# Kernel tuning notes

Measured on AMD Instinct MI355X. Metric: run time of the kernel, lower is better.

Reference implementation:

```python
import jax, jax.numpy as jnp
import numpy as np


def reference(x, edge_index, edge_attr, W, b):
    """PyG GCNConv: out = D^{-1/2} (A + I) D^{-1/2} X W + b.

    x: [N, Din] node features
    edge_index: [2, E] int (row=source, col=target)
    edge_attr: [E] edge weights
    W: [Din, Dout], b: [Dout]
    """
    N = x.shape[0]
    # add self-loops with weight 1 (PyG fill_value=1.0)
    loop = jnp.arange(N, dtype=edge_index.dtype)
    row = jnp.concatenate([edge_index[0], loop])
    col = jnp.concatenate([edge_index[1], loop])
    w = jnp.concatenate([edge_attr, jnp.ones((N,), dtype=edge_attr.dtype)])

    # symmetric normalization: norm_e = d[row]^-1/2 * w_e * d[col]^-1/2
    deg = jax.ops.segment_sum(w, col, num_segments=N)
    dis = jnp.where(deg > 0, jax.lax.rsqrt(jnp.where(deg > 0, deg, 1.0)), 0.0)
    norm = dis[row] * w * dis[col]

    # linear projection first (Din == Dout, cheaper either way), then
    # gather-scale-scatter aggregation at targets
    h = x @ W                                   # [N, Dout]
    msg = h[row] * norm[:, None]                # [E+N, Dout]
    out = jax.ops.segment_sum(msg, col, num_segments=N)  # [N, Dout]
    return out + b


def setup_inputs() -> dict:
    key = jax.random.key(0)
    k1, k2, k3, k4 = jax.random.split(key, 4)
    N, E, Din, Dout = 100000, 1600000, 128, 128
    x = jax.random.normal(k1, (N, Din), dtype=jnp.float32)
    edge_index = jax.random.randint(k2, (2, E), 0, N, dtype=jnp.int64)
    edge_attr = jax.random.uniform(k3, (E,), dtype=jnp.float32)
    # Glorot init like PyG Linear default
    W = jax.random.normal(k4, (Din, Dout), dtype=jnp.float32) * (1.0 / np.sqrt(Din))
    b = jnp.zeros((Dout,), dtype=jnp.float32)
    return {"x": x, "edge_index": edge_index, "edge_attr": edge_attr, "W": W, "b": b}
```

## Files before the change

kernel.cpp:

```cpp
#include <hip/hip_runtime.h>


#define ELEMS_PER_SCAN_BLOCK 4096
#define CHUNK 2048

typedef __attribute__((ext_vector_type(8))) short short8;
typedef __attribute__((ext_vector_type(4))) float f32x4;

__device__ inline unsigned short f2bf(float f) {
    unsigned u = __float_as_uint(f);
    u += 0x7fffu + ((u >> 16) & 1u);
    return (unsigned short)(u >> 16);
}
__device__ inline float bf_lo(unsigned u) { return __uint_as_float(u << 16); }
__device__ inline float bf_hi(unsigned u) { return __uint_as_float(u & 0xffff0000u); }

__global__ __launch_bounds__(256) void k_hist(const int* __restrict__ col,
                                              int* __restrict__ histg,
                                              int E, int NC, int NBLK) {
    __shared__ int lh[1024];
    int t = threadIdx.x, blk = blockIdx.x;
    for (int i = t; i < 1024; i += 256) lh[i] = 0;
    __syncthreads();
    int base = blk * CHUNK;
    #pragma unroll
    for (int i = 0; i < CHUNK / 256; ++i) {
        int e = base + i * 256 + t;
        if (e < E) atomicAdd(&lh[col[e] >> 7], 1);
    }
    __syncthreads();
    for (int b = t; b < NC; b += 256) histg[b * NBLK + blk] = lh[b];
}

__device__ inline int wave_incl_scan(int x, int lane) {
    #pragma unroll
    for (int d = 1; d < 64; d <<= 1) {
        int y = __shfl_up(x, d, 64);
        if (lane >= d) x += y;
    }
    return x;
}

__global__ void k_scan1(const int* __restrict__ in, int* __restrict__ out,
                        int* __restrict__ bsum, int M) {
    __shared__ int wsum[4];
    __shared__ int woff[4];
    int t = threadIdx.x, lane = t & 63, wid = t >> 6;
    int base = blockIdx.x * ELEMS_PER_SCAN_BLOCK + t * 16;
    int v[16];
    #pragma unroll
    for (int i = 0; i < 16; ++i) v[i] = (base + i < M) ? in[base + i] : 0;
    int run = 0;
    #pragma unroll
    for (int i = 0; i < 16; ++i) { int x = v[i]; v[i] = run; run += x; }
    int incl = wave_incl_scan(run, lane);
    int excl = incl - run;
    if (lane == 63) wsum[wid] = incl;
    __syncthreads();
    if (t == 0) {
        int r = 0;
        #pragma unroll
        for (int w = 0; w < 4; ++w) { int s = wsum[w]; woff[w] = r; r += s; }
        bsum[blockIdx.x] = r;
    }
    __syncthreads();
    int off = woff[wid] + excl;
    #pragma unroll
    for (int i = 0; i < 16; ++i)
        if (base + i < M) out[base + i] = v[i] + off;
}

__global__ void k_scan2(const int* __restrict__ bsum, int* __restrict__ boff, int NB) {
    __shared__ int wsum[4];
    __shared__ int woff[4];
    int t = threadIdx.x, lane = t & 63, wid = t >> 6;
    int x = (t < NB) ? bsum[t] : 0;
    int incl = wave_incl_scan(x, lane);
    int excl = incl - x;
    if (lane == 63) wsum[wid] = incl;
    __syncthreads();
    if (t == 0) {
        int r = 0;
        #pragma unroll
        for (int w = 0; w < 4; ++w) { int s = wsum[w]; woff[w] = r; r += s; }
    }
    __syncthreads();
    if (t < NB) boff[t] = woff[wid] + excl;
}

__global__ void k_scan3(int* __restrict__ arr, const int* __restrict__ boff, int M) {
    int t = threadIdx.x;
    int base = blockIdx.x * ELEMS_PER_SCAN_BLOCK + t * 16;
    int off = boff[blockIdx.x];
    #pragma unroll
    for (int i = 0; i < 16; ++i) {
        int idx = base + i;
        if (idx < M) arr[idx] += off;
    }
}

__global__ __launch_bounds__(256) void k_place(const int* __restrict__ row,
                                               const int* __restrict__ col,
                                               const float* __restrict__ wgt,
                                               const int* __restrict__ histg,
                                               int2* __restrict__ srw,
                                               int E, int NC, int NBLK) {
    __shared__ int lcnt[1024];
    __shared__ int gadj[1024];
    __shared__ int2 stage[CHUNK];
    __shared__ int sdst[CHUNK];
    __shared__ int wsum[4];
    __shared__ int woff[4];
    int t = threadIdx.x, blk = blockIdx.x;
    int lane = t & 63, wid = t >> 6;
    int base = blk * CHUNK;
    int nE = min(CHUNK, E - base);
    for (int b = t; b < 1024; b += 256) lcnt[b] = 0;
    __syncthreads();
    #pragma unroll
    for (int i = 0; i < CHUNK / 256; ++i) {
        int e = base + i * 256 + t;
        if (e < E) atomicAdd(&lcnt[col[e] >> 7], 1);
    }
    __syncthreads();
    int c4[4];
    int sum = 0;
    #pragma unroll
    for (int i = 0; i < 4; ++i) { int v = lcnt[t * 4 + i]; c4[i] = sum; sum += v; }
    int incl = wave_incl_scan(sum, lane);
    int excl = incl - sum;
    if (lane == 63) wsum[wid] = incl;
    __syncthreads();
    if (t == 0) {
        int r = 0;
        #pragma unroll
        for (int w = 0; w < 4; ++w) { int s = wsum[w]; woff[w] = r; r += s; }
    }
    __syncthreads();
    int tb = woff[wid] + excl;
    #pragma unroll
    for (int i = 0; i < 4; ++i) {
        int idx = t * 4 + i;
        int b0 = tb + c4[i];
        int gb = (idx < NC) ? histg[idx * NBLK + blk] : 0;
        gadj[idx] = gb - b0;
        lcnt[idx] = b0;
    }
    __syncthreads();
    #pragma unroll
    for (int i = 0; i < CHUNK / 256; ++i) {
        int e = base + i * 256 + t;
        if (e < E) {
            int c = col[e];
            int slot = atomicAdd(&lcnt[c >> 7], 1);
            stage[slot] = make_int2(((c & 127) << 17) | row[e], __float_as_int(wgt[e]));
            sdst[slot] = gadj[c >> 7] + slot;
        }
    }
    __syncthreads();
    for (int s_ = t; s_ < nE; s_ += 256) {
        srw[sdst[s_]] = stage[s_];
    }
}

__global__ __launch_bounds__(256) void k_fine(const int* __restrict__ histg,
                                              const int2* __restrict__ srw,
                                              int* __restrict__ rowptr,
                                              float* __restrict__ dis,
                                              int2* __restrict__ spack,
                                              int E, int N, int NC, int NBLK) {
    __shared__ int cnt128[128];
    __shared__ float degf[128];
    __shared__ int cur128[128];
    __shared__ int wtot[2];
    int t = threadIdx.x, b = blockIdx.x;
    int nb = b << 7;
    int start = histg[b * NBLK];
    int end = (b == NC - 1) ? E : histg[(b + 1) * NBLK];
    if (t < 128) { cnt128[t] = 0; degf[t] = 1.0f; }
    __syncthreads();
    for (int j = start + t; j < end; j += 256) {
        int2 s = srw[j];
        int c = s.x >> 17;
        atomicAdd(&cnt128[c], 1);
        atomicAdd(&degf[c], __int_as_float(s.y));
    }
    __syncthreads();
    int v = 0, incl = 0;
    if (t < 128) {
        v = cnt128[t];
        incl = wave_incl_scan(v, t & 63);
        if ((t & 63) == 63) wtot[t >> 6] = incl;
    }
    __syncthreads();
    if (t < 128) {
        int excl = incl - v + ((t >= 64) ? wtot[0] : 0);
        int p = start + excl;
        cur128[t] = p;
        int n = nb + t;
        if (n < N) {
            rowptr[n] = p;
            dis[n] = rsqrtf(degf[t]);
        }
    }
    if (t == 0 && b == NC - 1) rowptr[N] = E;
    __syncthreads();
    for (int j = start + t; j < end; j += 256) {
        int2 s = srw[j];
        int c = s.x >> 17;
        int pos = atomicAdd(&cur128[c], 1);
        spack[pos] = make_int2(s.x & 0x1FFFF, s.y);
    }
}

__global__ void k_wprep(const float* __restrict__ W, unsigned short* __restrict__ Wtg) {
    int n = blockIdx.x;
    int k = threadIdx.x;
    Wtg[n * 128 + k] = f2bf(W[k * 128 + n]);
}

__global__ __launch_bounds__(256) void k_gemm(const float* __restrict__ x,
                                              const unsigned short* __restrict__ Wtg,
                                              unsigned short* __restrict__ h, int N) {
    __shared__ short Xs[64][136];
    __shared__ short Ws[128][136];
    int t = threadIdx.x;
    int lane = t & 63, wid = t >> 6;
    int row0 = blockIdx.x * 64;
    {
        int r = t >> 2;
        int kseg = (t & 3) * 32;
        int gr = row0 + r;
        const float4* src = (const float4*)(x + (size_t)gr * 128 + kseg);
        #pragma unroll
        for (int i = 0; i < 4; ++i) {
            float4 v0 = make_float4(0.f, 0.f, 0.f, 0.f), v1 = v0;
            if (gr < N) { v0 = src[2 * i]; v1 = src[2 * i + 1]; }
            short8 p;
            p[0] = (short)f2bf(v0.x); p[1] = (short)f2bf(v0.y);
            p[2] = (short)f2bf(v0.z); p[3] = (short)f2bf(v0.w);
            p[4] = (short)f2bf(v1.x); p[5] = (short)f2bf(v1.y);
            p[6] = (short)f2bf(v1.z); p[7] = (short)f2bf(v1.w);
            *(short8*)&Xs[r][kseg + 8 * i] = p;
        }
    }
    {
        int n = t >> 1;
        int seg = (t & 1) * 64;
        const short* wsrc = (const short*)Wtg + n * 128 + seg;
        #pragma unroll
        for (int i = 0; i < 8; ++i)
            *(short8*)&Ws[n][seg + 8 * i] = *(const short8*)(wsrc + 8 * i);
    }
    __syncthreads();

    int q = lane >> 4;
    int m = lane & 15;
    f32x4 acc[8];
    #pragma unroll
    for (int tde = 0; tde < 8; ++tde) acc[tde] = (f32x4){0.f, 0.f, 0.f, 0.f};
    #pragma unroll
    for (int kc = 0; kc < 128; kc += 32) {
        short8 af = *(const short8*)&Xs[wid * 16 + m][kc + q * 8];
        #pragma unroll
        for (int tde = 0; tde < 8; ++tde) {
            short8 bf = *(const short8*)&Ws[tde * 16 + m][kc + q * 8];
            acc[tde] = __builtin_amdgcn_mfma_f32_16x16x32_bf16(af, bf, acc[tde], 0, 0, 0);
        }
    }
    #pragma unroll
    for (int r = 0; r < 4; ++r) {
        int grow = row0 + wid * 16 + q * 4 + r;
        if (grow < N) {
            #pragma unroll
            for (int tde = 0; tde < 8; ++tde)
                h[(size_t)grow * 128 + tde * 16 + m] = f2bf(acc[tde][r]);
        }
    }
}

__global__ __launch_bounds__(256) void k_gather(const unsigned int* __restrict__ hb,
                                                const float* __restrict__ dis,
                                                const int* __restrict__ rowptr,
                                                const long* __restrict__ spackl,
                                                const float* __restrict__ bias,
                                                float* __restrict__ out, int N) {
    int gid = blockIdx.x * blockDim.x + threadIdx.x;
    int node = gid >> 6;
    int lane = gid & 63;
    if (node >= N) return;
    node = __builtin_amdgcn_readfirstlane(node);

    float dn = dis[node];
    unsigned u = hb[(size_t)node * 64 + lane];
    float2 acc;
    acc.x = dn * bf_lo(u);
    acc.y = dn * bf_hi(u);

    int jb = rowptr[node], je = rowptr[node + 1];
    int j = jb;
    long q0, q1, q2, q3, q4, q5, q6, q7;
    if (j + 8 <= je) {
        q0 = __builtin_nontemporal_load(spackl + j);
        q1 = __builtin_nontemporal_load(spackl + j + 1);
        q2 = __builtin_nontemporal_load(spackl + j + 2);
        q3 = __builtin_nontemporal_load(spackl + j + 3);
        q4 = __builtin_nontemporal_load(spackl + j + 4);
        q5 = __builtin_nontemporal_load(spackl + j + 5);
        q6 = __builtin_nontemporal_load(spackl + j + 6);
        q7 = __builtin_nontemporal_load(spackl + j + 7);
    }
    for (; j + 8 <= je; j += 8) {
        int r0 = __builtin_amdgcn_readfirstlane((int)q0);
        int r1 = __builtin_amdgcn_readfirstlane((int)q1);
        int r2 = __builtin_amdgcn_readfirstlane((int)q2);
        int r3 = __builtin_amdgcn_readfirstlane((int)q3);
        int r4 = __builtin_amdgcn_readfirstlane((int)q4);
        int r5 = __builtin_amdgcn_readfirstlane((int)q5);
        int r6 = __builtin_amdgcn_readfirstlane((int)q6);
        int r7 = __builtin_amdgcn_readfirstlane((int)q7);
        unsigned u0 = hb[(size_t)r0 * 64 + lane];
        unsigned u1 = hb[(size_t)r1 * 64 + lane];
        unsigned u2 = hb[(size_t)r2 * 64 + lane];
        unsigned u3 = hb[(size_t)r3 * 64 + lane];
        unsigned u4 = hb[(size_t)r4 * 64 + lane];
        unsigned u5 = hb[(size_t)r5 * 64 + lane];
        unsigned u6 = hb[(size_t)r6 * 64 + lane];
        unsigned u7 = hb[(size_t)r7 * 64 + lane];
        int jn = (j + 16 <= je) ? j + 8 : j;
        long n0 = __builtin_nontemporal_load(spackl + jn);
        long n1 = __builtin_nontemporal_load(spackl + jn + 1);
        long n2 = __builtin_nontemporal_load(spackl + jn + 2);
        long n3 = __builtin_nontemporal_load(spackl + jn + 3);
        long n4 = __builtin_nontemporal_load(spackl + jn + 4);
        long n5 = __builtin_nontemporal_load(spackl + jn + 5);
        long n6 = __builtin_nontemporal_load(spackl + jn + 6);
        long n7 = __builtin_nontemporal_load(spackl + jn + 7);
        float a0 = dis[r0] * __uint_as_float((unsigned)((unsigned long)q0 >> 32));
        float a1 = dis[r1] * __uint_as_float((unsigned)((unsigned long)q1 >> 32));
        float a2 = dis[r2] * __uint_as_float((unsigned)((unsigned long)q2 >> 32));
        float a3 = dis[r3] * __uint_as_float((unsigned)((unsigned long)q3 >> 32));
        float a4 = dis[r4] * __uint_as_float((unsigned)((unsigned long)q4 >> 32));
        float a5 = dis[r5] * __uint_as_float((unsigned)((unsigned long)q5 >> 32));
        float a6 = dis[r6] * __uint_as_float((unsigned)((unsigned long)q6 >> 32));
        float a7 = dis[r7] * __uint_as_float((unsigned)((unsigned long)q7 >> 32));
        acc.x = fmaf(a0, bf_lo(u0), acc.x); acc.y = fmaf(a0, bf_hi(u0), acc.y);
        acc.x = fmaf(a1, bf_lo(u1), acc.x); acc.y = fmaf(a1, bf_hi(u1), acc.y);
        acc.x = fmaf(a2, bf_lo(u2), acc.x); acc.y = fmaf(a2, bf_hi(u2), acc.y);
        acc.x = fmaf(a3, bf_lo(u3), acc.x); acc.y = fmaf(a3, bf_hi(u3), acc.y);
        acc.x = fmaf(a4, bf_lo(u4), acc.x); acc.y = fmaf(a4, bf_hi(u4), acc.y);
        acc.x = fmaf(a5, bf_lo(u5), acc.x); acc.y = fmaf(a5, bf_hi(u5), acc.y);
        acc.x = fmaf(a6, bf_lo(u6), acc.x); acc.y = fmaf(a6, bf_hi(u6), acc.y);
        acc.x = fmaf(a7, bf_lo(u7), acc.x); acc.y = fmaf(a7, bf_hi(u7), acc.y);
        q0 = n0; q1 = n1; q2 = n2; q3 = n3; q4 = n4; q5 = n5; q6 = n6; q7 = n7;
    }
    for (; j < je; ++j) {
        long q = __builtin_nontemporal_load(spackl + j);
        int r = __builtin_amdgcn_readfirstlane((int)q);
        unsigned uu = hb[(size_t)r * 64 + lane];
        float a = dis[r] * __uint_as_float((unsigned)((unsigned long)q >> 32));
        acc.x = fmaf(a, bf_lo(uu), acc.x);
        acc.y = fmaf(a, bf_hi(uu), acc.y);
    }

    int c0 = lane * 2;
    float2 bv = *(const float2*)(bias + c0);
    float2 o;
    o.x = bv.x + dn * acc.x;
    o.y = bv.y + dn * acc.y;
    union { float2 f; double d; } cvt;
    cvt.f = o;
    __builtin_nontemporal_store(cvt.d, (double*)(out + (size_t)node * 128 + c0));
}

extern "C" void kernel_launch(void* const* d_in, const int* in_sizes, int n_in,
                              void* d_out, int out_size, void* d_ws, size_t ws_size,
                              hipStream_t stream) {
    const float* x     = (const float*)d_in[0];
    const int*   eidx  = (const int*)d_in[1];
    const float* eattr = (const float*)d_in[2];
    const float* W     = (const float*)d_in[3];
    const float* bias  = (const float*)d_in[4];
    int N = in_sizes[0] / 128;
    int E = in_sizes[2];
    const int* row = eidx;
    const int* col = eidx + E;

    int NC = (N + 127) >> 7;
    int NBLK = (E + CHUNK - 1) / CHUNK;

    char* p = (char*)d_ws;
    auto carve = [&](size_t bytes) {
        char* q = p;
        p += (bytes + 255) & ~(size_t)255;
        return q;
    };
    unsigned short* h   = (unsigned short*)carve((size_t)N * 128 * sizeof(unsigned short));
    unsigned short* Wtg = (unsigned short*)carve(128 * 128 * sizeof(unsigned short));
    float* dis    = (float*)carve((size_t)N * sizeof(float));
    int*   rowptr = (int*)carve((size_t)(N + 1) * sizeof(int));
    int*   histg  = (int*)carve((size_t)NC * NBLK * sizeof(int));
    int2*  srw    = (int2*)carve((size_t)E * sizeof(int2));
    int2*  spack  = (int2*)carve((size_t)E * sizeof(int2));
    int*   bsum   = (int*)carve(256 * sizeof(int));
    int*   boff   = (int*)carve(256 * sizeof(int));

    int M = NC * NBLK;
    int NBs = (M + ELEMS_PER_SCAN_BLOCK - 1) / ELEMS_PER_SCAN_BLOCK;

    k_hist<<<NBLK, 256, 0, stream>>>(col, histg, E, NC, NBLK);
    k_scan1<<<NBs, 256, 0, stream>>>(histg, histg, bsum, M);
    k_scan2<<<1, 256, 0, stream>>>(bsum, boff, NBs);
    k_scan3<<<NBs, 256, 0, stream>>>(histg, boff, M);
    k_place<<<NBLK, 256, 0, stream>>>(row, col, eattr, histg, srw, E, NC, NBLK);
    k_fine<<<NC, 256, 0, stream>>>(histg, srw, rowptr, dis, spack, E, N, NC, NBLK);
    k_wprep<<<128, 128, 0, stream>>>(W, Wtg);
    k_gemm<<<(N + 63) / 64, 256, 0, stream>>>(x, Wtg, h, N);
    {
        size_t threads = (size_t)N * 64;
        int blocks = (int)((threads + 255) / 256);
        k_gather<<<blocks, 256, 0, stream>>>((const unsigned int*)h, dis, rowptr,
                                             (const long*)spack, bias, (float*)d_out, N);
    }
}
```

Measured before the change: 270.2 us.

## Co-schedule GEMM blocks with CSR build kernels and fold scan and weight prep

The weight transpose and bf16 conversion move into the histogram kernel. The scan-offset add kernel is removed, and its block offsets are applied on the fly when the scanned histogram is read. Half of the GEMM tiles now run as extra blocks in the placement kernel and the other half in the fine-bucketing kernel, so the compute-bound projection overlaps with the memory- and atomic-bound CSR construction and the launch count drops. The fine kernel caches up to 3072 bucket entries in shared memory to avoid re-reading them from global memory. The union shared-memory layout raises per-block LDS, which may lower occupancy for the scatter phases.

```diff
diff --git a/kernel.cpp b/kernel.cpp
--- a/kernel.cpp
+++ b/kernel.cpp
@@ -2,6 +2,7 @@
 
 
 #define ELEMS_PER_SCAN_BLOCK 4096
+#define SCAN_SHIFT 12
 #define CHUNK 2048
 
 typedef __attribute__((ext_vector_type(8))) short short8;
@@ -15,11 +16,26 @@
 __device__ inline float bf_lo(unsigned u) { return __uint_as_float(u << 16); }
 __device__ inline float bf_hi(unsigned u) { return __uint_as_float(u & 0xffff0000u); }
 
+union SmemU {
+    struct { short Xs[64][136]; short Ws[128][136]; } g;
+    struct { int lcnt[1024]; int gadj[1024]; int2 stage[CHUNK]; int sdst[CHUNK];
+             int wsum[4]; int woff[4]; } p;
+    struct { int2 sbuf[3072]; int cnt128[128]; float degf[128]; int cur128[128];
+             int wtot[2]; } f;
+};
+
 __global__ __launch_bounds__(256) void k_hist(const int* __restrict__ col,
+                                              const float* __restrict__ W,
                                               int* __restrict__ histg,
+                                              unsigned short* __restrict__ Wtg,
                                               int E, int NC, int NBLK) {
     __shared__ int lh[1024];
     int t = threadIdx.x, blk = blockIdx.x;
+    if (blk < 64) {
+        int n = blk * 2 + (t >> 7);
+        int k = t & 127;
+        Wtg[n * 128 + k] = f2bf(W[k * 128 + n]);
+    }
     for (int i = t; i < 1024; i += 256) lh[i] = 0;
     __syncthreads();
     int base = blk * CHUNK;
@@ -88,145 +104,11 @@
     if (t < NB) boff[t] = woff[wid] + excl;
 }
 
-__global__ void k_scan3(int* __restrict__ arr, const int* __restrict__ boff, int M) {
-    int t = threadIdx.x;
-    int base = blockIdx.x * ELEMS_PER_SCAN_BLOCK + t * 16;
-    int off = boff[blockIdx.x];
-    #pragma unroll
-    for (int i = 0; i < 16; ++i) {
-        int idx = base + i;
-        if (idx < M) arr[idx] += off;
-    }
-}
-
-__global__ __launch_bounds__(256) void k_place(const int* __restrict__ row,
-                                               const int* __restrict__ col,
-                                               const float* __restrict__ wgt,
-                                               const int* __restrict__ histg,
-                                               int2* __restrict__ srw,
-                                               int E, int NC, int NBLK) {
-    __shared__ int lcnt[1024];
-    __shared__ int gadj[1024];
-    __shared__ int2 stage[CHUNK];
-    __shared__ int sdst[CHUNK];
-    __shared__ int wsum[4];
-    __shared__ int woff[4];
-    int t = threadIdx.x, blk = blockIdx.x;
+__device__ __forceinline__ void gemm_body(SmemU& sm, const float* __restrict__ x,
+                                          const unsigned short* __restrict__ Wtg,
+                                          unsigned short* __restrict__ h,
+                                          int row0, int N, int t) {
     int lane = t & 63, wid = t >> 6;
-    int base = blk * CHUNK;
-    int nE = min(CHUNK, E - base);
-    for (int b = t; b < 1024; b += 256) lcnt[b] = 0;
-    __syncthreads();
-    #pragma unroll
-    for (int i = 0; i < CHUNK / 256; ++i) {
-        int e = base + i * 256 + t;
-        if (e < E) atomicAdd(&lcnt[col[e] >> 7], 1);
-    }
-    __syncthreads();
-    int c4[4];
-    int sum = 0;
-    #pragma unroll
-    for (int i = 0; i < 4; ++i) { int v = lcnt[t * 4 + i]; c4[i] = sum; sum += v; }
-    int incl = wave_incl_scan(sum, lane);
-    int excl = incl - sum;
-    if (lane == 63) wsum[wid] = incl;
-    __syncthreads();
-    if (t == 0) {
-        int r = 0;
-        #pragma unroll
-        for (int w = 0; w < 4; ++w) { int s = wsum[w]; woff[w] = r; r += s; }
-    }
-    __syncthreads();
-    int tb = woff[wid] + excl;
-    #pragma unroll
-    for (int i = 0; i < 4; ++i) {
-        int idx = t * 4 + i;
-        int b0 = tb + c4[i];
-        int gb = (idx < NC) ? histg[idx * NBLK + blk] : 0;
-        gadj[idx] = gb - b0;
-        lcnt[idx] = b0;
-    }
-    __syncthreads();
-    #pragma unroll
-    for (int i = 0; i < CHUNK / 256; ++i) {
-        int e = base + i * 256 + t;
-        if (e < E) {
-            int c = col[e];
-            int slot = atomicAdd(&lcnt[c >> 7], 1);
-            stage[slot] = make_int2(((c & 127) << 17) | row[e], __float_as_int(wgt[e]));
-            sdst[slot] = gadj[c >> 7] + slot;
-        }
-    }
-    __syncthreads();
-    for (int s_ = t; s_ < nE; s_ += 256) {
-        srw[sdst[s_]] = stage[s_];
-    }
-}
-
-__global__ __launch_bounds__(256) void k_fine(const int* __restrict__ histg,
-                                              const int2* __restrict__ srw,
-                                              int* __restrict__ rowptr,
-                                              float* __restrict__ dis,
-                                              int2* __restrict__ spack,
-                                              int E, int N, int NC, int NBLK) {
-    __shared__ int cnt128[128];
-    __shared__ float degf[128];
-    __shared__ int cur128[128];
-    __shared__ int wtot[2];
-    int t = threadIdx.x, b = blockIdx.x;
-    int nb = b << 7;
-    int start = histg[b * NBLK];
-    int end = (b == NC - 1) ? E : histg[(b + 1) * NBLK];
-    if (t < 128) { cnt128[t] = 0; degf[t] = 1.0f; }
-    __syncthreads();
-    for (int j = start + t; j < end; j += 256) {
-        int2 s = srw[j];
-        int c = s.x >> 17;
-        atomicAdd(&cnt128[c], 1);
-        atomicAdd(&degf[c], __int_as_float(s.y));
-    }
-    __syncthreads();
-    int v = 0, incl = 0;
-    if (t < 128) {
-        v = cnt128[t];
-        incl = wave_incl_scan(v, t & 63);
-        if ((t & 63) == 63) wtot[t >> 6] = incl;
-    }
-    __syncthreads();
-    if (t < 128) {
-        int excl = incl - v + ((t >= 64) ? wtot[0] : 0);
-        int p = start + excl;
-        cur128[t] = p;
-        int n = nb + t;
-        if (n < N) {
-            rowptr[n] = p;
-            dis[n] = rsqrtf(degf[t]);
-        }
-    }
-    if (t == 0 && b == NC - 1) rowptr[N] = E;
-    __syncthreads();
-    for (int j = start + t; j < end; j += 256) {
-        int2 s = srw[j];
-        int c = s.x >> 17;
-        int pos = atomicAdd(&cur128[c], 1);
-        spack[pos] = make_int2(s.x & 0x1FFFF, s.y);
-    }
-}
-
-__global__ void k_wprep(const float* __restrict__ W, unsigned short* __restrict__ Wtg) {
-    int n = blockIdx.x;
-    int k = threadIdx.x;
-    Wtg[n * 128 + k] = f2bf(W[k * 128 + n]);
-}
-
-__global__ __launch_bounds__(256) void k_gemm(const float* __restrict__ x,
-                                              const unsigned short* __restrict__ Wtg,
-                                              unsigned short* __restrict__ h, int N) {
-    __shared__ short Xs[64][136];
-    __shared__ short Ws[128][136];
-    int t = threadIdx.x;
-    int lane = t & 63, wid = t >> 6;
-    int row0 = blockIdx.x * 64;
     {
         int r = t >> 2;
         int kseg = (t & 3) * 32;
@@ -241,7 +123,7 @@
             p[2] = (short)f2bf(v0.z); p[3] = (short)f2bf(v0.w);
             p[4] = (short)f2bf(v1.x); p[5] = (short)f2bf(v1.y);
             p[6] = (short)f2bf(v1.z); p[7] = (short)f2bf(v1.w);
-            *(short8*)&Xs[r][kseg + 8 * i] = p;
+            *(short8*)&sm.g.Xs[r][kseg + 8 * i] = p;
         }
     }
     {
@@ -250,7 +132,7 @@
         const short* wsrc = (const short*)Wtg + n * 128 + seg;
         #pragma unroll
         for (int i = 0; i < 8; ++i)
-            *(short8*)&Ws[n][seg + 8 * i] = *(const short8*)(wsrc + 8 * i);
+            *(short8*)&sm.g.Ws[n][seg + 8 * i] = *(const short8*)(wsrc + 8 * i);
     }
     __syncthreads();
 
@@ -261,10 +143,10 @@
     for (int tde = 0; tde < 8; ++tde) acc[tde] = (f32x4){0.f, 0.f, 0.f, 0.f};
     #pragma unroll
     for (int kc = 0; kc < 128; kc += 32) {
-        short8 af = *(const short8*)&Xs[wid * 16 + m][kc + q * 8];
+        short8 af = *(const short8*)&sm.g.Xs[wid * 16 + m][kc + q * 8];
         #pragma unroll
         for (int tde = 0; tde < 8; ++tde) {
-            short8 bf = *(const short8*)&Ws[tde * 16 + m][kc + q * 8];
+            short8 bf = *(const short8*)&sm.g.Ws[tde * 16 + m][kc + q * 8];
             acc[tde] = __builtin_amdgcn_mfma_f32_16x16x32_bf16(af, bf, acc[tde], 0, 0, 0);
         }
     }
@@ -276,6 +158,144 @@
             for (int tde = 0; tde < 8; ++tde)
                 h[(size_t)grow * 128 + tde * 16 + m] = f2bf(acc[tde][r]);
         }
+    }
+}
+
+__global__ __launch_bounds__(256) void k_pg(const int* __restrict__ row,
+                                            const int* __restrict__ col,
+                                            const float* __restrict__ wgt,
+                                            const int* __restrict__ histg,
+                                            const int* __restrict__ boff,
+                                            int2* __restrict__ srw,
+                                            const float* __restrict__ x,
+                                            const unsigned short* __restrict__ Wtg,
+                                            unsigned short* __restrict__ h,
+                                            int E, int N, int NC, int NBLK) {
+    __shared__ SmemU sm;
+    int t = threadIdx.x;
+    if ((int)blockIdx.x >= NBLK) {
+        gemm_body(sm, x, Wtg, h, ((int)blockIdx.x - NBLK) * 64, N, t);
+        return;
+    }
+    int blk = blockIdx.x;
+    int lane = t & 63, wid = t >> 6;
+    int base = blk * CHUNK;
+    int nE = min(CHUNK, E - base);
+    for (int b = t; b < 1024; b += 256) sm.p.lcnt[b] = 0;
+    __syncthreads();
+    #pragma unroll
+    for (int i = 0; i < CHUNK / 256; ++i) {
+        int e = base + i * 256 + t;
+        if (e < E) atomicAdd(&sm.p.lcnt[col[e] >> 7], 1);
+    }
+    __syncthreads();
+    int c4[4];
+    int sum = 0;
+    #pragma unroll
+    for (int i = 0; i < 4; ++i) { int v = sm.p.lcnt[t * 4 + i]; c4[i] = sum; sum += v; }
+    int incl = wave_incl_scan(sum, lane);
+    int excl = incl - sum;
+    if (lane == 63) sm.p.wsum[wid] = incl;
+    __syncthreads();
+    if (t == 0) {
+        int r = 0;
+        #pragma unroll
+        for (int w = 0; w < 4; ++w) { int s = sm.p.wsum[w]; sm.p.woff[w] = r; r += s; }
+    }
+    __syncthreads();
+    int tb = sm.p.woff[wid] + excl;
+    __syncthreads();
+    #pragma unroll
+    for (int i = 0; i < 4; ++i) {
+        int idx = t * 4 + i;
+        int b0 = tb + c4[i];
+        int gb = 0;
+        if (idx < NC) {
+            int g = idx * NBLK + blk;
+            gb = histg[g] + boff[g >> SCAN_SHIFT];
+        }
+        sm.p.gadj[idx] = gb - b0;
+        sm.p.lcnt[idx] = b0;
+    }
+    __syncthreads();
+    #pragma unroll
+    for (int i = 0; i < CHUNK / 256; ++i) {
+        int e = base + i * 256 + t;
+        if (e < E) {
+            int c = col[e];
+            int slot = atomicAdd(&sm.p.lcnt[c >> 7], 1);
+            sm.p.stage[slot] = make_int2(((c & 127) << 17) | row[e], __float_as_int(wgt[e]));
+            sm.p.sdst[slot] = sm.p.gadj[c >> 7] + slot;
+        }
+    }
+    __syncthreads();
+    for (int s_ = t; s_ < nE; s_ += 256) {
+        srw[sm.p.sdst[s_]] = sm.p.stage[s_];
+    }
+}
+
+__global__ __launch_bounds__(256) void k_fg(const int* __restrict__ histg,
+                                            const int* __restrict__ boff,
+                                            const int2* __restrict__ srw,
+                                            int* __restrict__ rowptr,
+                                            float* __restrict__ dis,
+                                            int2* __restrict__ spack,
+                                            const float* __restrict__ x,
+                                            const unsigned short* __restrict__ Wtg,
+                                            unsigned short* __restrict__ h,
+                                            int E, int N, int NC, int NBLK, int GB1) {
+    __shared__ SmemU sm;
+    int t = threadIdx.x;
+    if ((int)blockIdx.x >= NC) {
+        gemm_body(sm, x, Wtg, h, (GB1 + (int)blockIdx.x - NC) * 64, N, t);
+        return;
+    }
+    int b = blockIdx.x;
+    int nb = b << 7;
+    int g0 = b * NBLK;
+    int start = histg[g0] + boff[g0 >> SCAN_SHIFT];
+    int end;
+    if (b == NC - 1) end = E;
+    else {
+        int g1 = (b + 1) * NBLK;
+        end = histg[g1] + boff[g1 >> SCAN_SHIFT];
+    }
+    int cnt = end - start;
+    int NL = min(cnt, 3072);
+    if (t < 128) { sm.f.cnt128[t] = 0; sm.f.degf[t] = 1.0f; }
+    __syncthreads();
+    for (int j = t; j < cnt; j += 256) {
+        int2 s = srw[start + j];
+        if (j < NL) sm.f.sbuf[j] = s;
+        int c = s.x >> 17;
+        atomicAdd(&sm.f.cnt128[c], 1);
+        atomicAdd(&sm.f.degf[c], __int_as_float(s.y));
+    }
+    __syncthreads();
+    int v = 0, incl = 0;
+    if (t < 128) {
+        v = sm.f.cnt128[t];
+        incl = wave_incl_scan(v, t & 63);
+        if ((t & 63) == 63) sm.f.wtot[t >> 6] = incl;
+    }
+    __syncthreads();
+    if (t < 128) {
+        int excl = incl - v + ((t >= 64) ? sm.f.wtot[0] : 0);
+        int p = start + excl;
+        sm.f.cur128[t] = p;
+        int n = nb + t;
+        if (n < N) {
+            rowptr[n] = p;
+            dis[n] = rsqrtf(sm.f.degf[t]);
+        }
+    }
+    if (t == 0 && b == NC - 1) rowptr[N] = E;
+    __syncthreads();
+    for (int j = t; j < cnt; j += 256) {
+        int2 s = (j < NL) ? sm.f.sbuf[j] : srw[start + j];
+        int c = s.x >> 17;
+        int pos = atomicAdd(&sm.f.cur128[c], 1);
+        spack[pos] = make_int2(s.x & 0x1FFFF, s.y);
     }
 }
 
@@ -408,14 +428,17 @@
     int M = NC * NBLK;
     int NBs = (M + ELEMS_PER_SCAN_BLOCK - 1) / ELEMS_PER_SCAN_BLOCK;
 
-    k_hist<<<NBLK, 256, 0, stream>>>(col, histg, E, NC, NBLK);
+    int GB  = (N + 63) / 64;
+    int GB1 = GB / 2;
+    int GB2 = GB - GB1;
+
+    k_hist<<<NBLK, 256, 0, stream>>>(col, W, histg, Wtg, E, NC, NBLK);
     k_scan1<<<NBs, 256, 0, stream>>>(histg, histg, bsum, M);
     k_scan2<<<1, 256, 0, stream>>>(bsum, boff, NBs);
-    k_scan3<<<NBs, 256, 0, stream>>>(histg, boff, M);
-    k_place<<<NBLK, 256, 0, stream>>>(row, col, eattr, histg, srw, E, NC, NBLK);
-    k_fine<<<NC, 256, 0, stream>>>(histg, srw, rowptr, dis, spack, E, N, NC, NBLK);
-    k_wprep<<<128, 128, 0, stream>>>(W, Wtg);
-    k_gemm<<<(N + 63) / 64, 256, 0, stream>>>(x, Wtg, h, N);
+    k_pg<<<NBLK + GB1, 256, 0, stream>>>(row, col, eattr, histg, boff, srw,
+                                         x, Wtg, h, E, N, NC, NBLK);
+    k_fg<<<NC + GB2, 256, 0, stream>>>(histg, boff, srw, rowptr, dis, spack,
+                                       x, Wtg, h, E, N, NC, NBLK, GB1);
     {
         size_t threads = (size_t)N * 64;
         int blocks = (int)((threads + 255) / 256);
```

Result: faster. 261.0 us (-3.4%).
